# Performance work log

Hardware: AMD Instinct MI355X
Metric: run time of the kernel (lower is better)

The kernel has to match this reference:

```python
import jax, jax.numpy as jnp
import numpy as np

N_PATCHES = 14
HIDDEN_D = 768
N_HEADS = 12
D_HEAD = HIDDEN_D // N_HEADS
OUT_D = 1000
IMG = 224
C = 3
PS = IMG // N_PATCHES  # 16
SEQ = N_PATCHES * N_PATCHES + 1  # 197
INPUT_D = C * PS * PS  # 768
EPS = 1e-5


def positional_embeddings(s, d):
    i = jnp.arange(s, dtype=jnp.float32)[:, None]
    j = jnp.arange(d, dtype=jnp.float32)[None, :]
    even = jnp.sin(i / jnp.power(10000.0, j / d))
    odd = jnp.cos(i / jnp.power(10000.0, (j - 1.0) / d))
    return jnp.where(jnp.arange(d)[None, :] % 2 == 0, even, odd)


def layernorm_2d(x, g, b):
    # torch nn.LayerNorm((S, D)): normalize over last two dims jointly, biased var
    mu = jnp.mean(x, axis=(-2, -1), keepdims=True)
    var = jnp.var(x, axis=(-2, -1), keepdims=True)
    return (x - mu) * jax.lax.rsqrt(var + EPS) * g + b


def setup_inputs() -> dict:
    key = jax.random.key(0)
    ks = jax.random.split(key, 16)
    s = 0.02
    return {
        "images": jax.random.normal(ks[0], (64, C, IMG, IMG), jnp.float32),
        "W_map": jax.random.normal(ks[1], (INPUT_D, HIDDEN_D), jnp.float32) * s,
        "b_map": jnp.zeros((HIDDEN_D,), jnp.float32),
        "cls_tok": jax.random.uniform(ks[2], (1, HIDDEN_D), jnp.float32),
        "ln1_g": jnp.ones((SEQ, HIDDEN_D), jnp.float32),
        "ln1_b": jnp.zeros((SEQ, HIDDEN_D), jnp.float32),
        "Wq": jax.random.normal(ks[3], (N_HEADS, D_HEAD, D_HEAD), jnp.float32) * s,
        "bq": jnp.zeros((N_HEADS, D_HEAD), jnp.float32),
        "Wk": jax.random.normal(ks[4], (N_HEADS, D_HEAD, D_HEAD), jnp.float32) * s,
        "bk": jnp.zeros((N_HEADS, D_HEAD), jnp.float32),
        "Wv": jax.random.normal(ks[5], (N_HEADS, D_HEAD, D_HEAD), jnp.float32) * s,
        "bv": jnp.zeros((N_HEADS, D_HEAD), jnp.float32),
        "ln2_g": jnp.ones((SEQ, HIDDEN_D), jnp.float32),
        "ln2_b": jnp.zeros((SEQ, HIDDEN_D), jnp.float32),
        "W_enc": jax.random.normal(ks[6], (HIDDEN_D, HIDDEN_D), jnp.float32) * s,
        "b_enc": jnp.zeros((HIDDEN_D,), jnp.float32),
        "W_out": jax.random.normal(ks[7], (HIDDEN_D, OUT_D), jnp.float32) * s,
        "b_out": jnp.zeros((OUT_D,), jnp.float32),
    }


def reference(images, W_map, b_map, cls_tok, ln1_g, ln1_b, Wq, bq, Wk, bk, Wv, bv,
              ln2_g, ln2_b, W_enc, b_enc, W_out, b_out):
    n = images.shape[0]
    # patchify: [N,C,H,W] -> [N, np*np, C*ps*ps], patch flattened in (C,ph,pw) order
    p = images.reshape(n, C, N_PATCHES, PS, N_PATCHES, PS)
    patches = p.transpose(0, 2, 4, 1, 3, 5).reshape(n, N_PATCHES * N_PATCHES, INPUT_D)

    tokens = patches @ W_map + b_map  # [N, np^2, D]
    cls = jnp.broadcast_to(cls_tok[None], (n, 1, HIDDEN_D))
    tokens = jnp.concatenate([cls, tokens], axis=1)  # [N, S, D]
    tokens = tokens + positional_embeddings(SEQ, HIDDEN_D)[None]

    # MSA on ln1(tokens), vectorized over batch and heads
    x = layernorm_2d(tokens, ln1_g, ln1_b)
    xh = x.reshape(n, SEQ, N_HEADS, D_HEAD)  # split hidden into heads
    q = jnp.einsum('bshd,hde->bshe', xh, Wq) + bq[None, None]
    k = jnp.einsum('bshd,hde->bshe', xh, Wk) + bk[None, None]
    v = jnp.einsum('bshd,hde->bshe', xh, Wv) + bv[None, None]
    scores = jnp.einsum('bshe,bthe->bhst', q, k) / np.sqrt(D_HEAD).astype(np.float32)
    attn = jax.nn.softmax(scores, axis=-1)  # [B,H,S,S]
    msa = jnp.einsum('bhst,bthe->bshe', attn, v).reshape(n, SEQ, HIDDEN_D)

    out = tokens + msa
    out = out + jax.nn.relu(layernorm_2d(out, ln2_g, ln2_b) @ W_enc + b_enc)
    cls_out = out[:, 0]  # [N, D]
    return jax.nn.softmax(cls_out @ W_out + b_out, axis=-1)
```

## Files before the change

### kernel.cpp

```cpp
#include <hip/hip_runtime.h>
#include <math.h>

#define SEQL 197
#define HD 768
#define NH 12
#define DHD 64
#define BATCH 64
#define OUTD 1000

typedef unsigned short ushort_t;
typedef __attribute__((ext_vector_type(8))) short bf16x8;
typedef __attribute__((ext_vector_type(4))) float f32x4;

static __device__ __forceinline__ unsigned short f2bf(float f) {
    union { float f; unsigned u; } v; v.f = f;
    unsigned r = v.u + 0x7fff + ((v.u >> 16) & 1);
    return (unsigned short)(r >> 16);
}

static __device__ __forceinline__ void gload16(const ushort_t* g, ushort_t* l) {
    __builtin_amdgcn_global_load_lds(
        (const __attribute__((address_space(1))) unsigned int*)g,
        (__attribute__((address_space(3))) unsigned int*)l, 16, 0, 0);
}

__global__ void k_init(const float* __restrict__ cls_tok, float* __restrict__ pos,
                       float* __restrict__ tok, float* __restrict__ stats) {
    int i = blockIdx.x * 256 + threadIdx.x;
    if (i < SEQL * HD) {
        int s = i / HD, d = i % HD;
        float f = (float)(d & ~1);
        float r = powf(10000.0f, -f / (float)HD);
        float a = (float)s * r;
        pos[i] = (d & 1) ? cosf(a) : sinf(a);
    } else {
        int j = i - SEQL * HD;
        if (j < BATCH * HD) {
            int b = j / HD, e = j % HD;
            float v = cls_tok[e] + ((e & 1) ? 1.0f : 0.0f);
            tok[(b * SEQL) * HD + e] = v;
            float sv = v, qv = v * v;
#pragma unroll
            for (int off = 32; off > 0; off >>= 1) {
                sv += __shfl_down(sv, off);
                qv += __shfl_down(qv, off);
            }
            if ((threadIdx.x & 63) == 0) {
                atomicAdd(&stats[2 * b], sv);
                atomicAdd(&stats[2 * b + 1], qv);
            }
        }
    }
}

__global__ void k_cvtAll(const float* __restrict__ W_map, const float* __restrict__ W_enc,
                         const float* __restrict__ Wq, const float* __restrict__ Wk,
                         const float* __restrict__ Wv,
                         ushort_t* __restrict__ WmT, ushort_t* __restrict__ WeT,
                         ushort_t* __restrict__ wt, float* __restrict__ stats) {
    int idx = blockIdx.x * 256 + threadIdx.x;
    if (blockIdx.x == 0 && threadIdx.x < 256) stats[threadIdx.x] = 0.f;
    if (idx < 2 * 147456) {
        const float* W = (idx < 147456) ? W_map : W_enc;
        ushort_t* WT   = (idx < 147456) ? WmT : WeT;
        int i = (idx < 147456) ? idx : idx - 147456;
        int k = i / 192, nq = i % 192;
        float4 w = *(const float4*)&W[k * 768 + nq * 4];
        WT[(nq * 4 + 0) * 768 + k] = f2bf(w.x);
        WT[(nq * 4 + 1) * 768 + k] = f2bf(w.y);
        WT[(nq * 4 + 2) * 768 + k] = f2bf(w.z);
        WT[(nq * 4 + 3) * 768 + k] = f2bf(w.w);
    } else {
        int i = idx - 2 * 147456;
        if (i < 36864) {
            int dq = i & 15;
            int e  = (i >> 4) & 63;
            int h  = (i >> 10) % 12;
            int pj = i / 12288;
            const float* W = (pj == 0) ? Wq : (pj == 1) ? Wk : Wv;
            ushort4 o;
            o.x = f2bf(W[(h * 64 + dq * 4 + 0) * 64 + e]);
            o.y = f2bf(W[(h * 64 + dq * 4 + 1) * 64 + e]);
            o.z = f2bf(W[(h * 64 + dq * 4 + 2) * 64 + e]);
            o.w = f2bf(W[(h * 64 + dq * 4 + 3) * 64 + e]);
            *(ushort4*)&wt[(size_t)((pj * 12 + h) * 64 + e) * 64 + dq * 4] = o;
        }
    }
}

__global__ void k_prep_patches(const float* __restrict__ img, ushort_t* __restrict__ Ae) {
    int idx = blockIdx.x * 256 + threadIdx.x;
    int m = idx / 192, kq = idx % 192;
    int k0 = kq * 4;
    int c = k0 >> 8, rem = k0 & 255, ir = rem >> 4, jc = rem & 15;
    int b = m / 196, pi = m % 196;
    int pr = pi / 14, pc = pi % 14;
    float4 v = *(const float4*)&img[((b * 3 + c) * 224 + pr * 16 + ir) * 224 + pc * 16 + jc];
    ushort4 o;
    o.x = f2bf(v.x); o.y = f2bf(v.y); o.z = f2bf(v.z); o.w = f2bf(v.w);
    *(ushort4*)&Ae[m * 768 + k0] = o;
}

template <int MODE>
__launch_bounds__(256)
__global__ void k_gemm_bf16(const ushort_t* __restrict__ A, const ushort_t* __restrict__ Bt,
                            const float* __restrict__ bias, const float* __restrict__ pos,
                            float* __restrict__ out, int Mtot, float* __restrict__ stats) {
    __shared__ ushort_t As[128 * 64];
    __shared__ ushort_t Bs[128 * 64];
    __shared__ float redS[4][4];
    const int m0 = blockIdx.x * 128;
    const int n0 = blockIdx.y * 128;
    const int tid = threadIdx.x;
    const int lane = tid & 63, wave = tid >> 6;
    const int wm = wave >> 1, wn = wave & 1;

    f32x4 acc[4][4];
#pragma unroll
    for (int i = 0; i < 4; ++i)
#pragma unroll
        for (int j = 0; j < 4; ++j)
#pragma unroll
            for (int r = 0; r < 4; ++r) acc[i][j][r] = 0.f;

    for (int kt = 0; kt < 12; ++kt) {
        const int k0 = kt * 64;
#pragma unroll
        for (int t = 0; t < 4; ++t) {
            int c = (wave << 2) | t;
            int o = c * 1024 + lane * 16;
            int row = o >> 7;
            int inner = o & 127;
            int col = (inner ^ ((row & 7) << 4)) >> 1;
            gload16(&A[(size_t)(m0 + row) * 768 + k0 + col], &As[c * 512]);
            gload16(&Bt[(size_t)(n0 + row) * 768 + k0 + col], &Bs[c * 512]);
        }
        __syncthreads();
#pragma unroll
        for (int ks = 0; ks < 2; ++ks) {
            const int cbyte = ks * 64 + (lane >> 4) * 16;
            bf16x8 af[4], bf[4];
#pragma unroll
            for (int mi = 0; mi < 4; ++mi) {
                int row = wm * 64 + mi * 16 + (lane & 15);
                af[mi] = *(const bf16x8*)((const char*)As + row * 128 + (cbyte ^ ((row & 7) << 4)));
            }
#pragma unroll
            for (int ni = 0; ni < 4; ++ni) {
                int n = wn * 64 + ni * 16 + (lane & 15);
                bf[ni] = *(const bf16x8*)((const char*)Bs + n * 128 + (cbyte ^ ((n & 7) << 4)));
            }
#pragma unroll
            for (int mi = 0; mi < 4; ++mi)
#pragma unroll
                for (int ni = 0; ni < 4; ++ni)
                    acc[mi][ni] = __builtin_amdgcn_mfma_f32_16x16x32_bf16(af[mi], bf[ni], acc[mi][ni], 0, 0, 0);
        }
        __syncthreads();
    }

    const int colb = n0 + wn * 64 + (lane & 15);
    const int rowb = m0 + wm * 64 + (lane >> 4) * 4;
    float s_lo = 0.f, q_lo = 0.f, s_hi = 0.f, q_hi = 0.f;
    const int bA = m0 / 196;
    const int mSplit = (bA + 1) * 196;
#pragma unroll
    for (int ni = 0; ni < 4; ++ni) {
        const int n = colb + ni * 16;
        const float bn = bias[n];
#pragma unroll
        for (int mi = 0; mi < 4; ++mi) {
#pragma unroll
            for (int r = 0; r < 4; ++r) {
                int m = rowb + mi * 16 + r;
                if (MODE == 0) {
                    int b = m / 196, s = 1 + m % 196;
                    float oval = acc[mi][ni][r] + bn + pos[s * HD + n];
                    out[((b * SEQL) + s) * HD + n] = oval;
                    if (m < mSplit) { s_lo += oval; q_lo += oval * oval; }
                    else            { s_hi += oval; q_hi += oval * oval; }
                } else {
                    if (m < Mtot) {
                        float* p = &out[(size_t)m * HD + n];
                        *p = *p + fmaxf(acc[mi][ni][r] + bn, 0.f);
                    }
                }
            }
        }
    }
    if (MODE == 0) {
#pragma unroll
        for (int off = 32; off > 0; off >>= 1) {
            s_lo += __shfl_down(s_lo, off);
            q_lo += __shfl_down(q_lo, off);
            s_hi += __shfl_down(s_hi, off);
            q_hi += __shfl_down(q_hi, off);
        }
        if (lane == 0) {
            redS[wave][0] = s_lo; redS[wave][1] = q_lo;
            redS[wave][2] = s_hi; redS[wave][3] = q_hi;
        }
        __syncthreads();
        if (tid == 0) {
            float a0 = 0.f, a1 = 0.f, a2 = 0.f, a3 = 0.f;
#pragma unroll
            for (int i = 0; i < 4; ++i) {
                a0 += redS[i][0]; a1 += redS[i][1];
                a2 += redS[i][2]; a3 += redS[i][3];
            }
            atomicAdd(&stats[2 * bA], a0);
            atomicAdd(&stats[2 * bA + 1], a1);
            int bB = bA + 1;
            if (bB < BATCH) {
                atomicAdd(&stats[2 * bB], a2);
                atomicAdd(&stats[2 * bB + 1], a3);
            }
        }
    }
}

__launch_bounds__(512, 2)
__global__ void k_qkvattn(const float* __restrict__ tok, float* __restrict__ stats,
                          const float* __restrict__ g1, const float* __restrict__ b1,
                          const ushort_t* __restrict__ wt,
                          const float* __restrict__ bq, const float* __restrict__ bk,
                          const float* __restrict__ bv, float* __restrict__ out) {
    const int h = blockIdx.x, b = blockIdx.y;
    __shared__ __attribute__((aligned(16))) ushort_t sm[32768];
    __shared__ float rS[8], rS2[8];
    const int tid = threadIdx.x;
    const int wave = tid >> 6, lane = tid & 63;
    const int l16 = lane & 15, l4 = lane >> 4;
    const int r0 = wave * 32;
    const float inv_n = 1.0f / (float)(SEQL * HD);
    const float S1_ = stats[b * 2], S2_ = stats[b * 2 + 1];
    const float mu = S1_ * inv_n;
    const float rsg = rsqrtf(S2_ * inv_n - mu * mu + 1e-5f);
    ushort_t* A16 = sm;
    ushort_t* B16 = sm + 16384;

    {
        const int row = tid >> 1, hw = tid & 1;
        if (row < SEQL) {
            const float* tp = &tok[((size_t)b * SEQL + row) * HD + h * 64 + hw * 32];
            const float* gp = &g1[(size_t)row * HD + h * 64 + hw * 32];
            const float* bp = &b1[(size_t)row * HD + h * 64 + hw * 32];
#pragma unroll
            for (int g = 0; g < 4; ++g) {
                float4 t0 = *(const float4*)&tp[g * 8];
                float4 t1 = *(const float4*)&tp[g * 8 + 4];
                float4 ga = *(const float4*)&gp[g * 8];
                float4 gb = *(const float4*)&gp[g * 8 + 4];
                float4 ba = *(const float4*)&bp[g * 8];
                float4 bb = *(const float4*)&bp[g * 8 + 4];
                bf16x8 o;
                o[0] = (short)f2bf((t0.x - mu) * rsg * ga.x + ba.x);
                o[1] = (short)f2bf((t0.y - mu) * rsg * ga.y + ba.y);
                o[2] = (short)f2bf((t0.z - mu) * rsg * ga.z + ba.z);
                o[3] = (short)f2bf((t0.w - mu) * rsg * ga.w + ba.w);
                o[4] = (short)f2bf((t1.x - mu) * rsg * gb.x + bb.x);
                o[5] = (short)f2bf((t1.y - mu) * rsg * gb.y + bb.y);
                o[6] = (short)f2bf((t1.z - mu) * rsg * gb.z + bb.z);
                o[7] = (short)f2bf((t1.w - mu) * rsg * gb.w + bb.w);
                int pc = (hw * 32 + g * 8) ^ ((row & 7) << 3);
                *(bf16x8*)&A16[row * 64 + pc] = o;
            }
        } else {
            bf16x8 z;
#pragma unroll
            for (int j = 0; j < 8; ++j) z[j] = 0;
#pragma unroll
            for (int g = 0; g < 4; ++g) {
                int pc = (hw * 32 + g * 8) ^ ((row & 7) << 3);
                *(bf16x8*)&A16[row * 64 + pc] = z;
            }
        }
    }

    bf16x8 af[2][2];
#pragma unroll
    for (int mi = 0; mi < 2; ++mi)
#pragma unroll
        for (int kk = 0; kk < 2; ++kk) {
            int row = r0 + mi * 16 + l16;
            af[mi][kk] = *(const bf16x8*)&A16[row * 64 + ((kk * 32 + l4 * 8) ^ ((row & 7) << 3))];
        }

#define PROJ_ACC(PJ, ACC)                                                                      \
    {                                                                                          \
        _Pragma("unroll") for (int ni = 0; ni < 4; ++ni) {                                     \
            const ushort_t* wr = &wt[(size_t)(((PJ) * 12 + h) * 64 + ni * 16 + l16) * 64];     \
            bf16x8 w0 = *(const bf16x8*)&wr[l4 * 8];                                           \
            bf16x8 w1 = *(const bf16x8*)&wr[32 + l4 * 8];                                      \
            _Pragma("unroll") for (int mi = 0; mi < 2; ++mi) {                                 \
                ACC[mi][ni] = __builtin_amdgcn_mfma_f32_16x16x32_bf16(af[mi][0], w0, ACC[mi][ni], 0, 0, 0); \
                ACC[mi][ni] = __builtin_amdgcn_mfma_f32_16x16x32_bf16(af[mi][1], w1, ACC[mi][ni], 0, 0, 0); \
            }                                                                                  \
        }                                                                                      \
    }

    f32x4 acc[2][4];
#define ZERO_ACC                                                                               \
    _Pragma("unroll") for (int mi = 0; mi < 2; ++mi)                                           \
        _Pragma("unroll") for (int ni = 0; ni < 4; ++ni) {                                     \
            acc[mi][ni][0] = 0.f; acc[mi][ni][1] = 0.f; acc[mi][ni][2] = 0.f; acc[mi][ni][3] = 0.f; }

    ZERO_ACC;
    PROJ_ACC(0, acc);
#pragma unroll
    for (int ni = 0; ni < 4; ++ni) {
        float bn = bq[h * 64 + ni * 16 + l16];
#pragma unroll
        for (int mi = 0; mi < 2; ++mi)
#pragma unroll
            for (int r = 0; r < 4; ++r) {
                int row = r0 + mi * 16 + l4 * 4 + r;
                A16[row * 64 + ((ni * 16 + l16) ^ ((row & 7) << 3))] = f2bf(acc[mi][ni][r] + bn);
            }
    }
    bf16x8 qa[2][2];
#pragma unroll
    for (int mi = 0; mi < 2; ++mi)
#pragma unroll
        for (int kk = 0; kk < 2; ++kk) {
            int row = r0 + mi * 16 + l16;
            qa[mi][kk] = *(const bf16x8*)&A16[row * 64 + ((kk * 32 + l4 * 8) ^ ((row & 7) << 3))];
        }

    ZERO_ACC;
    PROJ_ACC(1, acc);
#pragma unroll
    for (int ni = 0; ni < 4; ++ni) {
        float bn = bk[h * 64 + ni * 16 + l16];
#pragma unroll
        for (int mi = 0; mi < 2; ++mi)
#pragma unroll
            for (int r = 0; r < 4; ++r) {
                int t = r0 + mi * 16 + l4 * 4 + r;
                A16[t * 64 + ((ni * 16 + l16) ^ ((t & 7) << 3))] = f2bf(acc[mi][ni][r] + bn);
            }
    }

    ZERO_ACC;
    PROJ_ACC(2, acc);
#pragma unroll
    for (int ni = 0; ni < 4; ++ni) {
        float bn = bv[h * 64 + ni * 16 + l16];
#pragma unroll
        for (int mi = 0; mi < 2; ++mi) {
            int t4 = r0 + mi * 16 + l4 * 4;
            int e = ni * 16 + l16;
            ushort4 pkt;
            pkt.x = f2bf(acc[mi][ni][0] + bn);
            pkt.y = f2bf(acc[mi][ni][1] + bn);
            pkt.z = f2bf(acc[mi][ni][2] + bn);
            pkt.w = f2bf(acc[mi][ni][3] + bn);
            *(ushort4*)&B16[e * 256 + (t4 ^ ((e & 7) << 3))] = pkt;
        }
    }

    __syncthreads();

    f32x4 sa[2][16];
#pragma unroll
    for (int ni = 0; ni < 16; ++ni) {
        int t = ni * 16 + l16;
        bf16x8 k0 = *(const bf16x8*)&A16[t * 64 + ((l4 * 8) ^ ((t & 7) << 3))];
        bf16x8 k1 = *(const bf16x8*)&A16[t * 64 + ((32 + l4 * 8) ^ ((t & 7) << 3))];
#pragma unroll
        for (int mi = 0; mi < 2; ++mi) {
            f32x4 z;
            z[0] = 0.f; z[1] = 0.f; z[2] = 0.f; z[3] = 0.f;
            z = __builtin_amdgcn_mfma_f32_16x16x32_bf16(qa[mi][0], k0, z, 0, 0, 0);
            sa[mi][ni] = __builtin_amdgcn_mfma_f32_16x16x32_bf16(qa[mi][1], k1, z, 0, 0, 0);
        }
    }

    float l_s[2][4];
#pragma unroll
    for (int mi = 0; mi < 2; ++mi)
#pragma unroll
        for (int r = 0; r < 4; ++r) {
            float rsum = 0.f;
#pragma unroll
            for (int ni = 0; ni < 16; ++ni) {
                float p = (ni * 16 + l16 < SEQL) ? __expf(sa[mi][ni][r] * 0.125f) : 0.f;
                sa[mi][ni][r] = p;
                rsum += p;
            }
            rsum += __shfl_xor(rsum, 1);
            rsum += __shfl_xor(rsum, 2);
            rsum += __shfl_xor(rsum, 4);
            rsum += __shfl_xor(rsum, 8);
            l_s[mi][r] = rsum;
        }

    __syncthreads();

    f32x4 oacc[2][4];
#pragma unroll
    for (int mi = 0; mi < 2; ++mi)
#pragma unroll
        for (int ne = 0; ne < 4; ++ne) {
            oacc[mi][ne][0] = 0.f; oacc[mi][ne][1] = 0.f;
            oacc[mi][ne][2] = 0.f; oacc[mi][ne][3] = 0.f;
        }

    for (int c = 0; c < 4; ++c) {
#pragma unroll
        for (int j = 0; j < 4; ++j)
#pragma unroll
            for (int mi = 0; mi < 2; ++mi)
#pragma unroll
                for (int r = 0; r < 4; ++r) {
                    int row = r0 + mi * 16 + l4 * 4 + r;
                    A16[row * 64 + ((j * 16 + l16) ^ ((row & 7) << 3))] = f2bf(sa[mi][c * 4 + j][r]);
                }
        bf16x8 pa[2][2];
#pragma unroll
        for (int mi = 0; mi < 2; ++mi)
#pragma unroll
            for (int kk = 0; kk < 2; ++kk) {
                int row = r0 + mi * 16 + l16;
                pa[mi][kk] = *(const bf16x8*)&A16[row * 64 + ((kk * 32 + l4 * 8) ^ ((row & 7) << 3))];
            }
#pragma unroll
        for (int ne = 0; ne < 4; ++ne) {
            int e = ne * 16 + l16;
            bf16x8 v0 = *(const bf16x8*)&B16[e * 256 + ((c * 64 + l4 * 8) ^ ((e & 7) << 3))];
            bf16x8 v1 = *(const bf16x8*)&B16[e * 256 + ((c * 64 + 32 + l4 * 8) ^ ((e & 7) << 3))];
#pragma unroll
            for (int mi = 0; mi < 2; ++mi) {
                oacc[mi][ne] = __builtin_amdgcn_mfma_f32_16x16x32_bf16(pa[mi][0], v0, oacc[mi][ne], 0, 0, 0);
                oacc[mi][ne] = __builtin_amdgcn_mfma_f32_16x16x32_bf16(pa[mi][1], v1, oacc[mi][ne], 0, 0, 0);
            }
        }
    }

    __syncthreads();
    float* Osm = (float*)sm + wave * 2048;
#pragma unroll
    for (int mi = 0; mi < 2; ++mi)
#pragma unroll
        for (int r = 0; r < 4; ++r) {
            float inv = 1.0f / l_s[mi][r];
            int rl = mi * 16 + l4 * 4 + r;
#pragma unroll
            for (int ne = 0; ne < 4; ++ne)
                Osm[rl * 64 + ((ne * 16 + l16) ^ ((rl & 3) << 4))] = oacc[mi][ne][r] * inv;
        }
    float psum = 0.f, psq = 0.f;
#pragma unroll
    for (int it = 0; it < 8; ++it) {
        int rl = it * 4 + l4;
        int row = r0 + rl;
        if (row < SEQL) {
            size_t off = ((size_t)b * SEQL + row) * HD + h * 64 + l16 * 4;
            float4 ov = *(float4*)&Osm[rl * 64 + ((l16 * 4) ^ ((rl & 3) << 4))];
            float4 tv = *(const float4*)&tok[off];
            float4 o;
            o.x = ov.x + tv.x; o.y = ov.y + tv.y;
            o.z = ov.z + tv.z; o.w = ov.w + tv.w;
            *(float4*)&out[off] = o;
            psum += o.x + o.y + o.z + o.w;
            psq  += o.x * o.x + o.y * o.y + o.z * o.z + o.w * o.w;
        }
    }
#pragma unroll
    for (int off = 32; off > 0; off >>= 1) {
        psum += __shfl_down(psum, off);
        psq += __shfl_down(psq, off);
    }
    if (lane == 0) { rS[wave] = psum; rS2[wave] = psq; }
    __syncthreads();
    if (tid == 0) {
        float S = 0.f, S2 = 0.f;
#pragma unroll
        for (int i = 0; i < 8; ++i) { S += rS[i]; S2 += rS2[i]; }
        atomicAdd(&stats[128 + 2 * b], S);
        atomicAdd(&stats[129 + 2 * b], S2);
    }
#undef PROJ_ACC
#undef ZERO_ACC
}

__global__ void k_ln2apply(const float* __restrict__ outb, const float* __restrict__ stats,
                           const float* __restrict__ g2, const float* __restrict__ b2,
                           ushort_t* __restrict__ x) {
    int i = blockIdx.x * 256 + threadIdx.x;
    if (i >= BATCH * SEQL * HD / 4) return;
    int e4 = i * 4;
    int m = e4 / HD, kk = e4 % HD;
    int b = m / SEQL, s = m % SEQL;
    const float inv_n = 1.0f / (float)(SEQL * HD);
    float S = stats[128 + 2 * b], S2 = stats[129 + 2 * b];
    float mu = S * inv_n;
    float rsg = rsqrtf(S2 * inv_n - mu * mu + 1e-5f);
    float4 t = *(const float4*)&outb[e4];
    float4 g = *(const float4*)&g2[s * HD + kk];
    float4 bb = *(const float4*)&b2[s * HD + kk];
    ushort4 o;
    o.x = f2bf((t.x - mu) * rsg * g.x + bb.x);
    o.y = f2bf((t.y - mu) * rsg * g.y + bb.y);
    o.z = f2bf((t.z - mu) * rsg * g.z + bb.z);
    o.w = f2bf((t.w - mu) * rsg * g.w + bb.w);
    *(ushort4*)&x[e4] = o;
}

__launch_bounds__(256)
__global__ void k_head(const float* __restrict__ out, const float* __restrict__ Wo,
                       const float* __restrict__ bo, float* __restrict__ dout) {
    const int b = blockIdx.x, tid = threadIdx.x;
    __shared__ float cls[768];
    __shared__ float red[256];
    for (int i = tid; i < 192; i += 256)
        *(float4*)&cls[i * 4] = *(const float4*)&out[(b * SEQL) * HD + i * 4];
    __syncthreads();

    const int o0 = tid * 4;
    const bool ok = (o0 < OUTD);
    float4 acc = {0.f, 0.f, 0.f, 0.f};
    if (ok) {
        acc = *(const float4*)&bo[o0];
        for (int e = 0; e < 768; ++e) {
            float c = cls[e];
            float4 w = *(const float4*)&Wo[e * OUTD + o0];
            acc.x += c * w.x;
            acc.y += c * w.y;
            acc.z += c * w.z;
            acc.w += c * w.w;
        }
    }
    float mx = ok ? fmaxf(fmaxf(acc.x, acc.y), fmaxf(acc.z, acc.w)) : -INFINITY;
    red[tid] = mx;
    __syncthreads();
    for (int s = 128; s > 0; s >>= 1) {
        if (tid < s) red[tid] = fmaxf(red[tid], red[tid + s]);
        __syncthreads();
    }
    float M = red[0];
    __syncthreads();
    float4 p = {0.f, 0.f, 0.f, 0.f};
    float ls = 0.f;
    if (ok) {
        p.x = expf(acc.x - M);
        p.y = expf(acc.y - M);
        p.z = expf(acc.z - M);
        p.w = expf(acc.w - M);
        ls = p.x + p.y + p.z + p.w;
    }
    red[tid] = ls;
    __syncthreads();
    for (int s = 128; s > 0; s >>= 1) {
        if (tid < s) red[tid] += red[tid + s];
        __syncthreads();
    }
    float inv = 1.0f / red[0];
    if (ok) {
        p.x *= inv; p.y *= inv; p.z *= inv; p.w *= inv;
        *(float4*)&dout[b * OUTD + o0] = p;
    }
}

extern "C" void kernel_launch(void* const* d_in, const int* in_sizes, int n_in,
                              void* d_out, int out_size, void* d_ws, size_t ws_size,
                              hipStream_t stream) {
    const float* images  = (const float*)d_in[0];
    const float* W_map   = (const float*)d_in[1];
    const float* b_map   = (const float*)d_in[2];
    const float* cls_tok = (const float*)d_in[3];
    const float* ln1_g   = (const float*)d_in[4];
    const float* ln1_b   = (const float*)d_in[5];
    const float* Wq      = (const float*)d_in[6];
    const float* bq      = (const float*)d_in[7];
    const float* Wk      = (const float*)d_in[8];
    const float* bk      = (const float*)d_in[9];
    const float* Wv      = (const float*)d_in[10];
    const float* bv      = (const float*)d_in[11];
    const float* ln2_g   = (const float*)d_in[12];
    const float* ln2_b   = (const float*)d_in[13];
    const float* W_enc   = (const float*)d_in[14];
    const float* b_enc   = (const float*)d_in[15];
    const float* W_out   = (const float*)d_in[16];
    const float* b_out   = (const float*)d_in[17];

    float* ws = (float*)d_ws;
    const size_t BIG = (size_t)BATCH * SEQL * HD;

    float* pos   = ws;
    float* tok   = ws + 151552;
    float* outb  = tok + BIG;
    float* stats = outb + BIG;
    ushort_t* wtq = (ushort_t*)(stats + 256);
    ushort_t* Ae  = wtq + 147456;
    ushort_t* WmT = Ae + (size_t)12672 * 768;
    ushort_t* WeT = WmT + (size_t)768 * 768;
    ushort_t* Ae2 = Ae;

    k_cvtAll<<<1296, 256, 0, stream>>>(W_map, W_enc, Wq, Wk, Wv, WmT, WeT, wtq, stats);
    k_init<<<783, 256, 0, stream>>>(cls_tok, pos, tok, stats);
    k_prep_patches<<<9408, 256, 0, stream>>>(images, Ae);
    k_gemm_bf16<0><<<dim3(98, 6), 256, 0, stream>>>(Ae, WmT, b_map, pos, tok, 12544, stats);
    k_qkvattn<<<dim3(12, 64), 512, 0, stream>>>(tok, stats, ln1_g, ln1_b, wtq, bq, bk, bv, outb);
    k_ln2apply<<<9456, 256, 0, stream>>>(outb, stats, ln2_g, ln2_b, Ae2);
    k_gemm_bf16<1><<<dim3(99, 6), 256, 0, stream>>>(Ae2, WeT, b_enc, pos, outb, 12608, stats);
    k_head<<<64, 256, 0, stream>>>(outb, W_out, b_out, (float*)d_out);
}
```

Measured before the change: 263.5 us.

## Remap workgroups per XCD and split classifier head into atomic partial logits

Adds an XCD-aware block remapping so consecutive logical tiles of the GEMMs and the attention kernel land on the same XCD, meant to improve L2 reuse of shared A/B tiles across MI355X chiplets. The classifier head is split into a k_logits kernel with 4x64 blocks, each reducing a 192-wide slice of the hidden dimension with atomicAdd into a zeroed logits buffer, and a separate softmax kernel. The split raises parallelism over the 64-block serial head but adds an extra launch, atomics and a buffer that must be zeroed.

```diff
diff --git a/kernel.cpp b/kernel.cpp
--- a/kernel.cpp
+++ b/kernel.cpp
@@ -22,6 +22,12 @@
     __builtin_amdgcn_global_load_lds(
         (const __attribute__((address_space(1))) unsigned int*)g,
         (__attribute__((address_space(3))) unsigned int*)l, 16, 0, 0);
+}
+
+static __device__ __forceinline__ int xcd_chunk(int id, int nwg) {
+    int xcd = id & 7, ii = id >> 3;
+    int q = nwg >> 3, r = nwg & 7;
+    return (xcd < r) ? (xcd * (q + 1) + ii) : (r * (q + 1) + (xcd - r) * q + ii);
 }
 
 __global__ void k_init(const float* __restrict__ cls_tok, float* __restrict__ pos,
@@ -57,9 +63,11 @@
                          const float* __restrict__ Wq, const float* __restrict__ Wk,
                          const float* __restrict__ Wv,
                          ushort_t* __restrict__ WmT, ushort_t* __restrict__ WeT,
-                         ushort_t* __restrict__ wt, float* __restrict__ stats) {
+                         ushort_t* __restrict__ wt, float* __restrict__ stats,
+                         float* __restrict__ logits) {
     int idx = blockIdx.x * 256 + threadIdx.x;
     if (blockIdx.x == 0 && threadIdx.x < 256) stats[threadIdx.x] = 0.f;
+    if (idx < BATCH * OUTD) logits[idx] = 0.f;
     if (idx < 2 * 147456) {
         const float* W = (idx < 147456) ? W_map : W_enc;
         ushort_t* WT   = (idx < 147456) ? WmT : WeT;
@@ -105,12 +113,14 @@
 __launch_bounds__(256)
 __global__ void k_gemm_bf16(const ushort_t* __restrict__ A, const ushort_t* __restrict__ Bt,
                             const float* __restrict__ bias, const float* __restrict__ pos,
-                            float* __restrict__ out, int Mtot, float* __restrict__ stats) {
+                            float* __restrict__ out, int Mtot, float* __restrict__ stats,
+                            int nwg) {
     __shared__ ushort_t As[128 * 64];
     __shared__ ushort_t Bs[128 * 64];
     __shared__ float redS[4][4];
-    const int m0 = blockIdx.x * 128;
-    const int n0 = blockIdx.y * 128;
+    const int vid = xcd_chunk(blockIdx.x, nwg);
+    const int m0 = (vid / 6) * 128;
+    const int n0 = (vid % 6) * 128;
     const int tid = threadIdx.x;
     const int lane = tid & 63, wave = tid >> 6;
     const int wm = wave >> 1, wn = wave & 1;
@@ -225,7 +235,8 @@
                           const ushort_t* __restrict__ wt,
                           const float* __restrict__ bq, const float* __restrict__ bk,
                           const float* __restrict__ bv, float* __restrict__ out) {
-    const int h = blockIdx.x, b = blockIdx.y;
+    const int vid = xcd_chunk(blockIdx.x, 768);
+    const int h = vid % 12, b = vid / 12;
     __shared__ __attribute__((aligned(16))) ushort_t sm[32768];
     __shared__ float rS[8], rS2[8];
     const int tid = threadIdx.x;
@@ -508,28 +519,46 @@
 }
 
 __launch_bounds__(256)
-__global__ void k_head(const float* __restrict__ out, const float* __restrict__ Wo,
-                       const float* __restrict__ bo, float* __restrict__ dout) {
+__global__ void k_logits(const float* __restrict__ out, const float* __restrict__ Wo,
+                         float* __restrict__ logits) {
+    const int eg = blockIdx.x, b = blockIdx.y, tid = threadIdx.x;
+    __shared__ float cls[192];
+    if (tid < 48)
+        *(float4*)&cls[tid * 4] = *(const float4*)&out[(size_t)(b * SEQL) * HD + eg * 192 + tid * 4];
+    __syncthreads();
+    const int o0 = tid * 4;
+    if (o0 < OUTD) {
+        float4 acc = {0.f, 0.f, 0.f, 0.f};
+        const float* wbase = &Wo[(size_t)eg * 192 * OUTD + o0];
+#pragma unroll 4
+        for (int e = 0; e < 192; ++e) {
+            float c = cls[e];
+            float4 w = *(const float4*)&wbase[(size_t)e * OUTD];
+            acc.x += c * w.x;
+            acc.y += c * w.y;
+            acc.z += c * w.z;
+            acc.w += c * w.w;
+        }
+        atomicAdd(&logits[b * OUTD + o0 + 0], acc.x);
+        atomicAdd(&logits[b * OUTD + o0 + 1], acc.y);
+        atomicAdd(&logits[b * OUTD + o0 + 2], acc.z);
+        atomicAdd(&logits[b * OUTD + o0 + 3], acc.w);
+    }
+}
+
+__launch_bounds__(256)
+__global__ void k_head_sm(const float* __restrict__ logits, const float* __restrict__ bo,
+                          float* __restrict__ dout) {
     const int b = blockIdx.x, tid = threadIdx.x;
-    __shared__ float cls[768];
     __shared__ float red[256];
-    for (int i = tid; i < 192; i += 256)
-        *(float4*)&cls[i * 4] = *(const float4*)&out[(b * SEQL) * HD + i * 4];
-    __syncthreads();
-
     const int o0 = tid * 4;
     const bool ok = (o0 < OUTD);
     float4 acc = {0.f, 0.f, 0.f, 0.f};
     if (ok) {
-        acc = *(const float4*)&bo[o0];
-        for (int e = 0; e < 768; ++e) {
-            float c = cls[e];
-            float4 w = *(const float4*)&Wo[e * OUTD + o0];
-            acc.x += c * w.x;
-            acc.y += c * w.y;
-            acc.z += c * w.z;
-            acc.w += c * w.w;
-        }
+        float4 lg = *(const float4*)&logits[b * OUTD + o0];
+        float4 bb = *(const float4*)&bo[o0];
+        acc.x = lg.x + bb.x; acc.y = lg.y + bb.y;
+        acc.z = lg.z + bb.z; acc.w = lg.w + bb.w;
     }
     float mx = ok ? fmaxf(fmaxf(acc.x, acc.y), fmaxf(acc.z, acc.w)) : -INFINITY;
     red[tid] = mx;
@@ -595,14 +624,16 @@
     ushort_t* Ae  = wtq + 147456;
     ushort_t* WmT = Ae + (size_t)12672 * 768;
     ushort_t* WeT = WmT + (size_t)768 * 768;
+    float* logits = (float*)(WeT + (size_t)768 * 768);
     ushort_t* Ae2 = Ae;
 
-    k_cvtAll<<<1296, 256, 0, stream>>>(W_map, W_enc, Wq, Wk, Wv, WmT, WeT, wtq, stats);
+    k_cvtAll<<<1296, 256, 0, stream>>>(W_map, W_enc, Wq, Wk, Wv, WmT, WeT, wtq, stats, logits);
     k_init<<<783, 256, 0, stream>>>(cls_tok, pos, tok, stats);
     k_prep_patches<<<9408, 256, 0, stream>>>(images, Ae);
-    k_gemm_bf16<0><<<dim3(98, 6), 256, 0, stream>>>(Ae, WmT, b_map, pos, tok, 12544, stats);
-    k_qkvattn<<<dim3(12, 64), 512, 0, stream>>>(tok, stats, ln1_g, ln1_b, wtq, bq, bk, bv, outb);
+    k_gemm_bf16<0><<<588, 256, 0, stream>>>(Ae, WmT, b_map, pos, tok, 12544, stats, 588);
+    k_qkvattn<<<768, 512, 0, stream>>>(tok, stats, ln1_g, ln1_b, wtq, bq, bk, bv, outb);
     k_ln2apply<<<9456, 256, 0, stream>>>(outb, stats, ln2_g, ln2_b, Ae2);
-    k_gemm_bf16<1><<<dim3(99, 6), 256, 0, stream>>>(Ae2, WeT, b_enc, pos, outb, 12608, stats);
-    k_head<<<64, 256, 0, stream>>>(outb, W_out, b_out, (float*)d_out);
-}
+    k_gemm_bf16<1><<<594, 256, 0, stream>>>(Ae2, WeT, b_enc, pos, outb, 12608, stats, 594);
+    k_logits<<<dim3(4, 64), 256, 0, stream>>>(outb, W_out, logits);
+    k_head_sm<<<64, 256, 0, stream>>>(logits, b_out, (float*)d_out);
+}
```

After: 244.4 us. -7.2%, faster.
